# Optimization experiments

Hardware: AMD Instinct MI355X
Metric: run time of the kernel (lower is better)

## Reference

```python
import jax, jax.numpy as jnp
import numpy as np

DIM = 256
NUM_HEADS = 8
HEAD_DIM = DIM // NUM_HEADS      # 32
KEY_DIM = HEAD_DIM // 2          # attn_ratio=0.5 -> 16
SCALE = KEY_DIM ** -0.5
H_QKV = DIM + 2 * KEY_DIM * NUM_HEADS  # 512
EPS = 1e-5


def bn(y, gamma, beta, mean, var):
    # eval-mode BatchNorm2d over channel dim of NCHW
    inv = jax.lax.rsqrt(var + EPS) * gamma
    return y * inv[None, :, None, None] + (beta - mean * inv)[None, :, None, None]


def setup_inputs() -> dict:
    key = jax.random.key(0)
    ks = jax.random.split(key, 16)
    B, C, H, W = 16, DIM, 32, 32
    x = jax.random.normal(ks[0], (B, C, H, W), dtype=jnp.float32)
    w_qkv = jax.random.normal(ks[1], (H_QKV, C), dtype=jnp.float32) * 0.05
    g_qkv = jax.random.uniform(ks[2], (H_QKV,), minval=0.5, maxval=1.5)
    b_qkv = jax.random.normal(ks[3], (H_QKV,)) * 0.1
    m_qkv = jax.random.normal(ks[4], (H_QKV,)) * 0.1
    v_qkv = jax.random.uniform(ks[5], (H_QKV,), minval=0.5, maxval=1.5)
    w_pos = jax.random.normal(ks[6], (C, 1, 3, 3), dtype=jnp.float32) * 0.1
    g_pos = jax.random.uniform(ks[7], (C,), minval=0.5, maxval=1.5)
    b_pos = jax.random.normal(ks[8], (C,)) * 0.1
    m_pos = jax.random.normal(ks[9], (C,)) * 0.1
    v_pos = jax.random.uniform(ks[10], (C,), minval=0.5, maxval=1.5)
    w_proj = jax.random.normal(ks[11], (C, C), dtype=jnp.float32) * 0.05
    g_proj = jax.random.uniform(ks[12], (C,), minval=0.5, maxval=1.5)
    b_proj = jax.random.normal(ks[13], (C,)) * 0.1
    m_proj = jax.random.normal(ks[14], (C,)) * 0.1
    v_proj = jax.random.uniform(ks[15], (C,), minval=0.5, maxval=1.5)
    return dict(x=x, w_qkv=w_qkv, g_qkv=g_qkv, b_qkv=b_qkv, m_qkv=m_qkv, v_qkv=v_qkv,
                w_pos=w_pos, g_pos=g_pos, b_pos=b_pos, m_pos=m_pos, v_pos=v_pos,
                w_proj=w_proj, g_proj=g_proj, b_proj=b_proj, m_proj=m_proj, v_proj=v_proj)


def reference(x, w_qkv, g_qkv, b_qkv, m_qkv, v_qkv,
              w_pos, g_pos, b_pos, m_pos, v_pos,
              w_proj, g_proj, b_proj, m_proj, v_proj):
    B, C, H, W = x.shape
    N = H * W
    # 1x1 conv (no bias) + BN
    qkv = bn(jnp.einsum('bchw,oc->bohw', x, w_qkv), g_qkv, b_qkv, m_qkv, v_qkv)
    qkv = qkv.reshape(B, NUM_HEADS, 2 * KEY_DIM + HEAD_DIM, N)
    q = qkv[:, :, :KEY_DIM]                 # [B, h, kd, N]
    k = qkv[:, :, KEY_DIM:2 * KEY_DIM]      # [B, h, kd, N]
    v = qkv[:, :, 2 * KEY_DIM:]             # [B, h, hd, N]
    # attention: q^T k, softmax over keys
    scores = jnp.einsum('bhkn,bhkm->bhnm', q, k) * SCALE  # [B, h, N, N]
    attn = jax.nn.softmax(scores, axis=-1)
    # v @ attn^T -> [B, h, hd, N]
    attended = jnp.einsum('bhdn,bhmn->bhdm', v, attn).reshape(B, C, H, W)
    # depthwise 3x3 positional encoding on v + BN, residual add
    v_img = v.reshape(B, C, H, W)
    pos = jax.lax.conv_general_dilated(
        v_img, w_pos, window_strides=(1, 1), padding=((1, 1), (1, 1)),
        dimension_numbers=('NCHW', 'OIHW', 'NCHW'), feature_group_count=C)
    pos = bn(pos, g_pos, b_pos, m_pos, v_pos)
    out = attended + pos
    # final 1x1 projection + BN
    out = bn(jnp.einsum('bchw,oc->bohw', out, w_proj), g_proj, b_proj, m_proj, v_proj)
    return out
```

## Files before the change

kernel.cpp:

```cpp
#include <hip/hip_runtime.h>

typedef short v8s __attribute__((ext_vector_type(8)));
typedef float v4f __attribute__((ext_vector_type(4)));
typedef unsigned short u16;

#define NPIX 1024
#define EPS 1e-5f

__device__ __forceinline__ float bf2f(u16 u){
  return __uint_as_float(((unsigned)u) << 16);
}
__device__ __forceinline__ u16 f2bf(float f){
  unsigned b = __float_as_uint(f);
  b += 0x7FFF + ((b >> 16) & 1);
  return (u16)(b >> 16);
}
__device__ __forceinline__ unsigned cvtpk(float lo, float hi){
  unsigned r;
  asm("v_cvt_pk_bf16_f32 %0, %1, %2" : "=v"(r) : "v"(lo), "v"(hi));
  return r;
}
__device__ __forceinline__ float exp2n(float x){
#if __has_builtin(__builtin_amdgcn_exp2f)
  return __builtin_amdgcn_exp2f(x);
#else
  float r; asm("v_exp_f32 %0, %1" : "=v"(r) : "v"(x)); return r;
#endif
}

template<bool OUT_F32>
__global__ __launch_bounds__(256) void gemm_bn(
    const float* __restrict__ src, const float* __restrict__ W,
    const float* __restrict__ gam, const float* __restrict__ bet,
    const float* __restrict__ mu,  const float* __restrict__ var,
    u16* __restrict__ bout, float* __restrict__ fout, int Cin, int Cout)
{
  const int n0 = blockIdx.x * 64;
  const int o0 = blockIdx.y * 64;
  const int b  = blockIdx.z;
  const int tid = threadIdx.x;
  const int w = tid >> 6, lane = tid & 63, col = lane & 15, quad = lane >> 4;

  __shared__ u16 Alds[64 * 40];
  __shared__ u16 Blds[32 * 68];

  v4f acc[4];
#pragma unroll
  for (int i = 0; i < 4; i++) acc[i] = (v4f){0.f, 0.f, 0.f, 0.f};

  const int arow = tid >> 2, acs = (tid & 3) * 8;
  const int brow = tid >> 3, bns = (tid & 7) * 8;

  for (int k0 = 0; k0 < Cin; k0 += 32) {
    const float* pa = W + (size_t)(o0 + arow) * Cin + k0 + acs;
    float4 a0 = ((const float4*)pa)[0];
    float4 a1 = ((const float4*)pa)[1];
    const float* pb = src + ((size_t)b * Cin + k0 + brow) * NPIX + n0 + bns;
    float4 b0 = ((const float4*)pb)[0];
    float4 b1 = ((const float4*)pb)[1];

    __syncthreads();
    {
      uint4 pk;
      pk.x = cvtpk(a0.x, a0.y);
      pk.y = cvtpk(a0.z, a0.w);
      pk.z = cvtpk(a1.x, a1.y);
      pk.w = cvtpk(a1.z, a1.w);
      *(uint4*)(&Alds[arow * 40 + acs]) = pk;
    }
    {
      uint2 lo, hi;
      lo.x = cvtpk(b0.x, b0.y);
      lo.y = cvtpk(b0.z, b0.w);
      hi.x = cvtpk(b1.x, b1.y);
      hi.y = cvtpk(b1.z, b1.w);
      *(uint2*)(&Blds[brow * 68 + bns])     = lo;
      *(uint2*)(&Blds[brow * 68 + bns + 4]) = hi;
    }
    __syncthreads();

    v8s bf;
#pragma unroll
    for (int jj = 0; jj < 8; jj++)
      bf[jj] = (short)Blds[(quad * 8 + jj) * 68 + w * 16 + col];
#pragma unroll
    for (int mt = 0; mt < 4; mt++) {
      v8s af = *(const v8s*)(&Alds[(mt * 16 + col) * 40 + quad * 8]);
      acc[mt] = __builtin_amdgcn_mfma_f32_16x16x32_bf16(af, bf, acc[mt], 0, 0, 0);
    }
  }

  const int n = n0 + w * 16 + col;
#pragma unroll
  for (int mt = 0; mt < 4; mt++) {
#pragma unroll
    for (int r = 0; r < 4; r++) {
      int o = o0 + mt * 16 + quad * 4 + r;
      float inv = rsqrtf(var[o] + EPS) * gam[o];
      float val = acc[mt][r] * inv + (bet[o] - mu[o] * inv);
      size_t idx = (size_t)(b * Cout + o) * NPIX + n;
      if (OUT_F32) fout[idx] = val;
      else         bout[idx] = f2bf(val);
    }
  }
}

__global__ __launch_bounds__(256) void attn_mfma_kernel(
    const u16* __restrict__ qkv, float* __restrict__ att)
{
  const int qt = blockIdx.x, h = blockIdx.y, b = blockIdx.z;
  const int tid = threadIdx.x, w = tid >> 6, lane = tid & 63;
  const int col = lane & 15, quad = lane >> 4;
  const u16* base = qkv + (size_t)(b * 512 + h * 64) * NPIX;

  __shared__ u16 Kt[64 * 24];
  __shared__ u16 Vl[32 * 72];
  __shared__ u16 Pl[4][16 * 72];

  const int q0 = qt * 64 + w * 16;

  v8s qf = (v8s){0, 0, 0, 0, 0, 0, 0, 0};
  if (quad < 2) {
#pragma unroll
    for (int jj = 0; jj < 8; jj++) {
      int k = quad * 8 + jj;
      qf[jj] = (short)f2bf(bf2f(base[(size_t)k * NPIX + q0 + col])
                           * 0.36067376022224085f);
    }
  }

  float lsum = 0.f;
  v4f o_acc[2];
  o_acc[0] = (v4f){0, 0, 0, 0};
  o_acc[1] = (v4f){0, 0, 0, 0};

  const int kk4 = w * 4;
  const int vd = tid >> 3, vjs = (tid & 7) * 8;

  for (int j0 = 0; j0 < 1024; j0 += 64) {
    ushort4 t;
    t.x = base[(size_t)(16 + kk4 + 0) * NPIX + j0 + lane];
    t.y = base[(size_t)(16 + kk4 + 1) * NPIX + j0 + lane];
    t.z = base[(size_t)(16 + kk4 + 2) * NPIX + j0 + lane];
    t.w = base[(size_t)(16 + kk4 + 3) * NPIX + j0 + lane];
    uint4 vt = *(const uint4*)(base + (size_t)(32 + vd) * NPIX + j0 + vjs);

    __syncthreads();
    *(ushort4*)(&Kt[lane * 24 + kk4]) = t;
    *(uint4*)(&Vl[vd * 72 + vjs]) = vt;
    __syncthreads();

#pragma unroll
    for (int jt = 0; jt < 4; jt++) {
      v8s kf = (v8s){0, 0, 0, 0, 0, 0, 0, 0};
      if (quad < 2)
        kf = *(const v8s*)(&Kt[(jt * 16 + col) * 24 + quad * 8]);
      v4f z = (v4f){0, 0, 0, 0};
      v4f s = __builtin_amdgcn_mfma_f32_16x16x32_bf16(kf, qf, z, 0, 0, 0);
      float p0 = exp2n(s[0]);
      float p1 = exp2n(s[1]);
      float p2 = exp2n(s[2]);
      float p3 = exp2n(s[3]);
      lsum += (p0 + p1) + (p2 + p3);
      uint2 pk;
      pk.x = cvtpk(p0, p1);
      pk.y = cvtpk(p2, p3);
      *(uint2*)(&Pl[w][col * 72 + jt * 16 + quad * 4]) = pk;
    }

#pragma unroll
    for (int T = 0; T < 2; T++) {
      v8s pf = *(const v8s*)(&Pl[w][col * 72 + T * 32 + quad * 8]);
#pragma unroll
      for (int dt = 0; dt < 2; dt++) {
        v8s vf = *(const v8s*)(&Vl[(dt * 16 + col) * 72 + T * 32 + quad * 8]);
        o_acc[dt] = __builtin_amdgcn_mfma_f32_16x16x32_bf16(pf, vf, o_acc[dt], 0, 0, 0);
      }
    }
  }

  lsum += __shfl_xor(lsum, 16);
  lsum += __shfl_xor(lsum, 32);
  float ls[4];
#pragma unroll
  for (int r = 0; r < 4; r++) ls[r] = __shfl(lsum, quad * 4 + r);
#pragma unroll
  for (int dt = 0; dt < 2; dt++) {
    float4 pack;
    pack.x = o_acc[dt][0] * (1.f / ls[0]);
    pack.y = o_acc[dt][1] * (1.f / ls[1]);
    pack.z = o_acc[dt][2] * (1.f / ls[2]);
    pack.w = o_acc[dt][3] * (1.f / ls[3]);
    *(float4*)(&att[(size_t)(b * 256 + h * 32 + dt * 16 + col) * NPIX +
                    q0 + quad * 4]) = pack;
  }
}

__global__ __launch_bounds__(256) void conv_bn_add_center(
    const u16* __restrict__ qkv, float* __restrict__ att,
    const float* __restrict__ wpos,
    const float* __restrict__ gam, const float* __restrict__ bet,
    const float* __restrict__ mu,  const float* __restrict__ var)
{
  const int c = blockIdx.y, b = blockIdx.z;
  const int p = blockIdx.x * 256 + threadIdx.x;
  const int y = p >> 5, x = p & 31;
  const u16* v = qkv + (size_t)(b * 512 + (c >> 5) * 64 + 32 + (c & 31)) * NPIX;

  float accv = 0.f;
#pragma unroll
  for (int ky = 0; ky < 3; ky++) {
    int yy = y + ky - 1;
    if (yy < 0 || yy > 31) continue;
#pragma unroll
    for (int kx = 0; kx < 3; kx++) {
      int xx = x + kx - 1;
      if (xx < 0 || xx > 31) continue;
      accv += bf2f(v[yy * 32 + xx]) * wpos[c * 9 + ky * 3 + kx];
    }
  }
  float inv = rsqrtf(var[c] + EPS) * gam[c];
  float add = bet[c] - mu[c] * inv;
  size_t idx = (size_t)(b * 256 + c) * NPIX + p;
  att[idx] = accv * inv + add + att[idx];
}

extern "C" void kernel_launch(void* const* d_in, const int* in_sizes, int n_in,
                              void* d_out, int out_size, void* d_ws, size_t ws_size,
                              hipStream_t stream)
{
  (void)in_sizes; (void)n_in; (void)out_size; (void)ws_size;
  const float* x      = (const float*)d_in[0];
  const float* w_qkv  = (const float*)d_in[1];
  const float* g_qkv  = (const float*)d_in[2];
  const float* b_qkv  = (const float*)d_in[3];
  const float* m_qkv  = (const float*)d_in[4];
  const float* v_qkv  = (const float*)d_in[5];
  const float* w_pos  = (const float*)d_in[6];
  const float* g_pos  = (const float*)d_in[7];
  const float* b_pos  = (const float*)d_in[8];
  const float* m_pos  = (const float*)d_in[9];
  const float* v_pos  = (const float*)d_in[10];
  const float* w_proj = (const float*)d_in[11];
  const float* g_proj = (const float*)d_in[12];
  const float* b_proj = (const float*)d_in[13];
  const float* m_proj = (const float*)d_in[14];
  const float* v_proj = (const float*)d_in[15];

  u16*   qkv = (u16*)d_ws;
  float* att = (float*)d_in[0];

  gemm_bn<false><<<dim3(16, 8, 16), 256, 0, stream>>>(
      x, w_qkv, g_qkv, b_qkv, m_qkv, v_qkv, qkv, nullptr, 256, 512);
  attn_mfma_kernel<<<dim3(16, 8, 16), 256, 0, stream>>>(qkv, att);
  conv_bn_add_center<<<dim3(4, 256, 16), 256, 0, stream>>>(
      qkv, att, w_pos, g_pos, b_pos, m_pos, v_pos);
  gemm_bn<true><<<dim3(16, 4, 16), 256, 0, stream>>>(
      att, w_proj, g_proj, b_proj, m_proj, v_proj, nullptr,
      (float*)d_out, 256, 256);
}
```

Baseline: 187.6 us.

## Double-buffer LDS tiles and register-prefetch in GEMM and attention kernels

Both the GEMM+BN and attention kernels now keep two LDS buffers and prefetch the next tile's global data into registers while the current tile is computed, leaving one barrier per iteration instead of two. The GEMM also swaps operand roles so the source tile is stored transposed with packed 16-byte writes, hoists the BN scale and shift per output channel, and writes outputs as vectorized packed stores. This is meant to hide global load latency and cut barrier and scalar-store overhead, at the cost of more LDS and register use.

```diff
diff --git a/kernel.cpp b/kernel.cpp
--- a/kernel.cpp
+++ b/kernel.cpp
@@ -41,66 +41,81 @@
   const int tid = threadIdx.x;
   const int w = tid >> 6, lane = tid & 63, col = lane & 15, quad = lane >> 4;
 
-  __shared__ u16 Alds[64 * 40];
-  __shared__ u16 Blds[32 * 68];
+  __shared__ u16 Wl[2][64 * 40];
+  __shared__ u16 Sr[2][64 * 40];
+
+  const int o = o0 + w * 16 + col;
+  const float inv = rsqrtf(var[o] + EPS) * gam[o];
+  const float add = bet[o] - mu[o] * inv;
 
   v4f acc[4];
 #pragma unroll
   for (int i = 0; i < 4; i++) acc[i] = (v4f){0.f, 0.f, 0.f, 0.f};
 
-  const int arow = tid >> 2, acs = (tid & 3) * 8;
-  const int brow = tid >> 3, bns = (tid & 7) * 8;
-
-  for (int k0 = 0; k0 < Cin; k0 += 32) {
-    const float* pa = W + (size_t)(o0 + arow) * Cin + k0 + acs;
-    float4 a0 = ((const float4*)pa)[0];
-    float4 a1 = ((const float4*)pa)[1];
-    const float* pb = src + ((size_t)b * Cin + k0 + brow) * NPIX + n0 + bns;
-    float4 b0 = ((const float4*)pb)[0];
-    float4 b1 = ((const float4*)pb)[1];
-
-    __syncthreads();
+  const int so = tid >> 2, sks = (tid & 3) * 8;
+  const int sp = tid & 63, skg = (tid >> 6) * 8;
+
+  const float* wp = W + (size_t)(o0 + so) * Cin + sks;
+  const float* sb = src + (size_t)b * Cin * NPIX + n0 + sp;
+
+  float4 wa = ((const float4*)wp)[0];
+  float4 wb = ((const float4*)wp)[1];
+  float sv[8];
+#pragma unroll
+  for (int i = 0; i < 8; i++) sv[i] = sb[(size_t)(skg + i) * NPIX];
+
+  const int nt = Cin >> 5;
+  int cur = 0;
+  for (int t = 0; t < nt; ++t) {
     {
       uint4 pk;
-      pk.x = cvtpk(a0.x, a0.y);
-      pk.y = cvtpk(a0.z, a0.w);
-      pk.z = cvtpk(a1.x, a1.y);
-      pk.w = cvtpk(a1.z, a1.w);
-      *(uint4*)(&Alds[arow * 40 + acs]) = pk;
+      pk.x = cvtpk(wa.x, wa.y);
+      pk.y = cvtpk(wa.z, wa.w);
+      pk.z = cvtpk(wb.x, wb.y);
+      pk.w = cvtpk(wb.z, wb.w);
+      *(uint4*)(&Wl[cur][so * 40 + sks]) = pk;
     }
     {
-      uint2 lo, hi;
-      lo.x = cvtpk(b0.x, b0.y);
-      lo.y = cvtpk(b0.z, b0.w);
-      hi.x = cvtpk(b1.x, b1.y);
-      hi.y = cvtpk(b1.z, b1.w);
-      *(uint2*)(&Blds[brow * 68 + bns])     = lo;
-      *(uint2*)(&Blds[brow * 68 + bns + 4]) = hi;
+      uint4 pk;
+      pk.x = cvtpk(sv[0], sv[1]);
+      pk.y = cvtpk(sv[2], sv[3]);
+      pk.z = cvtpk(sv[4], sv[5]);
+      pk.w = cvtpk(sv[6], sv[7]);
+      *(uint4*)(&Sr[cur][sp * 40 + skg]) = pk;
+    }
+    if (t + 1 < nt) {
+      const float* wpn = wp + (t + 1) * 32;
+      wa = ((const float4*)wpn)[0];
+      wb = ((const float4*)wpn)[1];
+      const float* sbn = sb + (size_t)((t + 1) * 32 + skg) * NPIX;
+#pragma unroll
+      for (int i = 0; i < 8; i++) sv[i] = sbn[(size_t)i * NPIX];
     }
     __syncthreads();
 
-    v8s bf;
-#pragma unroll
-    for (int jj = 0; jj < 8; jj++)
-      bf[jj] = (short)Blds[(quad * 8 + jj) * 68 + w * 16 + col];
+    v8s bfrag = *(const v8s*)(&Wl[cur][(w * 16 + col) * 40 + quad * 8]);
 #pragma unroll
     for (int mt = 0; mt < 4; mt++) {
-      v8s af = *(const v8s*)(&Alds[(mt * 16 + col) * 40 + quad * 8]);
-      acc[mt] = __builtin_amdgcn_mfma_f32_16x16x32_bf16(af, bf, acc[mt], 0, 0, 0);
-    }
-  }
-
-  const int n = n0 + w * 16 + col;
+      v8s af = *(const v8s*)(&Sr[cur][(mt * 16 + col) * 40 + quad * 8]);
+      acc[mt] = __builtin_amdgcn_mfma_f32_16x16x32_bf16(af, bfrag, acc[mt], 0, 0, 0);
+    }
+    cur ^= 1;
+  }
+
+  const size_t orow = (size_t)(b * Cout + o) * NPIX + n0 + quad * 4;
 #pragma unroll
   for (int mt = 0; mt < 4; mt++) {
-#pragma unroll
-    for (int r = 0; r < 4; r++) {
-      int o = o0 + mt * 16 + quad * 4 + r;
-      float inv = rsqrtf(var[o] + EPS) * gam[o];
-      float val = acc[mt][r] * inv + (bet[o] - mu[o] * inv);
-      size_t idx = (size_t)(b * Cout + o) * NPIX + n;
-      if (OUT_F32) fout[idx] = val;
-      else         bout[idx] = f2bf(val);
+    float v0 = acc[mt][0] * inv + add;
+    float v1 = acc[mt][1] * inv + add;
+    float v2 = acc[mt][2] * inv + add;
+    float v3 = acc[mt][3] * inv + add;
+    if (OUT_F32) {
+      *(float4*)(&fout[orow + mt * 16]) = make_float4(v0, v1, v2, v3);
+    } else {
+      uint2 pk;
+      pk.x = cvtpk(v0, v1);
+      pk.y = cvtpk(v2, v3);
+      *(uint2*)(&bout[orow + mt * 16]) = pk;
     }
   }
 }
@@ -113,8 +128,8 @@
   const int col = lane & 15, quad = lane >> 4;
   const u16* base = qkv + (size_t)(b * 512 + h * 64) * NPIX;
 
-  __shared__ u16 Kt[64 * 24];
-  __shared__ u16 Vl[32 * 72];
+  __shared__ u16 Kt[2][64 * 24];
+  __shared__ u16 Vl[2][32 * 72];
   __shared__ u16 Pl[4][16 * 72];
 
   const int q0 = qt * 64 + w * 16;
@@ -137,24 +152,32 @@
   const int kk4 = w * 4;
   const int vd = tid >> 3, vjs = (tid & 7) * 8;
 
-  for (int j0 = 0; j0 < 1024; j0 += 64) {
-    ushort4 t;
-    t.x = base[(size_t)(16 + kk4 + 0) * NPIX + j0 + lane];
-    t.y = base[(size_t)(16 + kk4 + 1) * NPIX + j0 + lane];
-    t.z = base[(size_t)(16 + kk4 + 2) * NPIX + j0 + lane];
-    t.w = base[(size_t)(16 + kk4 + 3) * NPIX + j0 + lane];
-    uint4 vt = *(const uint4*)(base + (size_t)(32 + vd) * NPIX + j0 + vjs);
-
-    __syncthreads();
-    *(ushort4*)(&Kt[lane * 24 + kk4]) = t;
-    *(uint4*)(&Vl[vd * 72 + vjs]) = vt;
+  ushort4 kr;
+  kr.x = base[(size_t)(16 + kk4 + 0) * NPIX + lane];
+  kr.y = base[(size_t)(16 + kk4 + 1) * NPIX + lane];
+  kr.z = base[(size_t)(16 + kk4 + 2) * NPIX + lane];
+  kr.w = base[(size_t)(16 + kk4 + 3) * NPIX + lane];
+  uint4 vr = *(const uint4*)(base + (size_t)(32 + vd) * NPIX + vjs);
+
+  int cur = 0;
+  for (int t = 0; t < 16; ++t) {
+    *(ushort4*)(&Kt[cur][lane * 24 + kk4]) = kr;
+    *(uint4*)(&Vl[cur][vd * 72 + vjs]) = vr;
+    if (t < 15) {
+      const int j0n = (t + 1) * 64;
+      kr.x = base[(size_t)(16 + kk4 + 0) * NPIX + j0n + lane];
+      kr.y = base[(size_t)(16 + kk4 + 1) * NPIX + j0n + lane];
+      kr.z = base[(size_t)(16 + kk4 + 2) * NPIX + j0n + lane];
+      kr.w = base[(size_t)(16 + kk4 + 3) * NPIX + j0n + lane];
+      vr = *(const uint4*)(base + (size_t)(32 + vd) * NPIX + j0n + vjs);
+    }
     __syncthreads();
 
 #pragma unroll
     for (int jt = 0; jt < 4; jt++) {
       v8s kf = (v8s){0, 0, 0, 0, 0, 0, 0, 0};
       if (quad < 2)
-        kf = *(const v8s*)(&Kt[(jt * 16 + col) * 24 + quad * 8]);
+        kf = *(const v8s*)(&Kt[cur][(jt * 16 + col) * 24 + quad * 8]);
       v4f z = (v4f){0, 0, 0, 0};
       v4f s = __builtin_amdgcn_mfma_f32_16x16x32_bf16(kf, qf, z, 0, 0, 0);
       float p0 = exp2n(s[0]);
@@ -173,10 +196,11 @@
       v8s pf = *(const v8s*)(&Pl[w][col * 72 + T * 32 + quad * 8]);
 #pragma unroll
       for (int dt = 0; dt < 2; dt++) {
-        v8s vf = *(const v8s*)(&Vl[(dt * 16 + col) * 72 + T * 32 + quad * 8]);
+        v8s vf = *(const v8s*)(&Vl[cur][(dt * 16 + col) * 72 + T * 32 + quad * 8]);
         o_acc[dt] = __builtin_amdgcn_mfma_f32_16x16x32_bf16(pf, vf, o_acc[dt], 0, 0, 0);
       }
     }
+    cur ^= 1;
   }
 
   lsum += __shfl_xor(lsum, 16);
```

New measurement: 184.5 us. Within noise of the previous version (-1.7%).
